# Kernel tuning notes

Measured on AMD Instinct MI355X. Metric: run time of the kernel, lower is better.

Reference implementation:

```python
import jax, jax.numpy as jnp
import numpy as np

B, N, E, NREG, DIN, F = 16, 20000, 640000, 2000, 128, 32
NEG_SLOPE = 0.2  # PyG GATConv default negative_slope


def setup_inputs() -> dict:
    key = jax.random.key(0)
    ks = jax.random.split(key, 10)
    x = jax.random.normal(ks[0], (B, N, DIN), dtype=jnp.float32)
    edge_src = jnp.sort(jax.random.randint(ks[1], (E,), 0, NREG, dtype=jnp.int64))
    edge_dst = jax.random.randint(ks[2], (E,), 0, N, dtype=jnp.int64)
    edge_attr = jax.random.uniform(ks[3], (B, E, 1), dtype=jnp.float32)
    # GATConv parameters (heads=1, concat=False, edge_dim=1)
    W = jax.random.normal(ks[4], (DIN, F), dtype=jnp.float32) * 0.05   # lin (shared src/dst)
    att_src = jax.random.normal(ks[5], (F,), dtype=jnp.float32) * 0.1
    att_dst = jax.random.normal(ks[6], (F,), dtype=jnp.float32) * 0.1
    lin_edge = jax.random.normal(ks[7], (1, F), dtype=jnp.float32) * 0.1
    att_edge = jax.random.normal(ks[8], (F,), dtype=jnp.float32) * 0.1
    bias = jax.random.normal(ks[9], (F,), dtype=jnp.float32) * 0.01
    return {"x": x, "edge_attr": edge_attr, "W": W, "att_src": att_src,
            "att_dst": att_dst, "lin_edge": lin_edge, "att_edge": att_edge,
            "bias": bias, "edge_src": edge_src, "edge_dst": edge_dst}


def _gat_regulon(x, eattr, W, att_src, att_dst, lin_edge, att_edge, bias,
                 src, dst):
    # x: [N, DIN], eattr: [E, 1]; src/dst: [E] int (src < NREG, sorted)
    h = x @ W                                  # [N, F]
    a_src = h @ att_src                        # [N]
    a_dst = h @ att_dst                        # [N]
    # add_self_loops=True with fill_value='mean' for edge_attr
    loop_attr = jnp.broadcast_to(jnp.mean(eattr, axis=0, keepdims=True), (N, 1))
    eattr_full = jnp.concatenate([eattr, loop_attr], axis=0)         # [E+N, 1]
    sl = jnp.arange(N, dtype=src.dtype)
    src_f = jnp.concatenate([src, sl])                               # [E+N]
    dst_f = jnp.concatenate([dst, sl])                               # [E+N]
    a_edge = (eattr_full @ lin_edge) @ att_edge                      # [E+N]
    alpha = jax.nn.leaky_relu(a_src[src_f] + a_dst[dst_f] + a_edge, NEG_SLOPE)
    # segment softmax over destination nodes (self-loops => no empty segment)
    m = jax.ops.segment_max(alpha, dst_f, num_segments=N)
    ex = jnp.exp(alpha - m[dst_f])
    s = jax.ops.segment_sum(ex, dst_f, num_segments=N)
    coef = ex / s[dst_f]                                             # [E+N]
    rep = jax.ops.segment_sum(coef[:, None] * h[src_f], dst_f, num_segments=N)
    rep = rep + bias                                                 # [N, F]
    # fused regulon pooling: out[i] = rep[i] + sum_{(i->t) in E} rep[t]
    pooled = jax.ops.segment_sum(rep[dst], src, num_segments=NREG)   # [NREG, F]
    return rep[:NREG] + pooled


def reference(x, edge_attr, W, att_src, att_dst, lin_edge, att_edge, bias,
              edge_src, edge_dst):
    fn = jax.vmap(lambda xi, ei: _gat_regulon(xi, ei, W, att_src, att_dst,
                                              lin_edge, att_edge, bias,
                                              edge_src, edge_dst))
    return fn(x, edge_attr)                                          # [B, NREG, F]
```

## Files before the change

### kernel.cpp

```cpp
#include <hip/hip_runtime.h>
#include <math.h>

#define B    16
#define N    20000
#define E    640000
#define NREG 2000
#define DIN  128
#define F    32
#define NEG  0.2f
#define BF   (B * F)
#define NCHUNK 8
#define CS   2500

typedef unsigned int uint;

__device__ inline uint bf16pair(float a, float b) {
    uint ua = __float_as_uint(a); ua = (ua + 0x7fffu + ((ua >> 16) & 1u)) >> 16;
    uint ub = __float_as_uint(b); ub = (ub + 0x7fffu + ((ub >> 16) & 1u)) >> 16;
    return ua | (ub << 16);
}
__device__ inline float bf16lo(uint v) { return __uint_as_float(v << 16); }
__device__ inline float bf16hi(uint v) { return __uint_as_float(v & 0xffff0000u); }

__global__ void k_hist(const int* __restrict__ dst, int* __restrict__ counts) {
    int e = blockIdx.x * blockDim.x + threadIdx.x;
    int stride = gridDim.x * blockDim.x;
    for (; e < E; e += stride)
        atomicAdd(&counts[dst[e]], 1);
}

__global__ void k_roff(const int* __restrict__ esrc, int* __restrict__ roff) {
    int r = blockIdx.x * blockDim.x + threadIdx.x;
    if (r > NREG) return;
    int lo = 0, hi = E;
    while (lo < hi) {
        int mid = (lo + hi) >> 1;
        if (esrc[mid] < r) lo = mid + 1; else hi = mid;
    }
    roff[r] = lo;
}

__global__ void k_scan(const int* __restrict__ in, int* __restrict__ out, int n) {
    __shared__ int sh[1024];
    int t = threadIdx.x;
    int chunk = (n + 1023) / 1024;
    int lo = t * chunk;
    int hi = lo + chunk; if (hi > n) hi = n;
    int local = 0;
    for (int i = lo; i < hi; ++i) local += in[i];
    sh[t] = local;
    __syncthreads();
    for (int d = 1; d < 1024; d <<= 1) {
        int v = (t >= d) ? sh[t - d] : 0;
        __syncthreads();
        sh[t] += v;
        __syncthreads();
    }
    int run = (t == 0) ? 0 : sh[t - 1];
    for (int i = lo; i < hi; ++i) { out[i] = run; run += in[i]; }
    if (t == 1023) out[n] = sh[1023];
}

__global__ void k_scatter(const int* __restrict__ src, const int* __restrict__ dst,
                          const int* __restrict__ off, int* __restrict__ cursor,
                          int* __restrict__ csr_src, int* __restrict__ pos_of_e) {
    int e = blockIdx.x * blockDim.x + threadIdx.x;
    int stride = gridDim.x * blockDim.x;
    for (; e < E; e += stride) {
        int d = dst[e];
        int pos = off[d] + atomicAdd(&cursor[d], 1);
        csr_src[pos] = src[e];
        pos_of_e[e] = pos;
    }
}

__global__ __launch_bounds__(256) void k_bucket(const int* __restrict__ edst,
                                                const int* __restrict__ roff,
                                                int* __restrict__ boff,
                                                int* __restrict__ pe_dst) {
    __shared__ int cnt[NCHUNK], pref[NCHUNK], cur[NCHUNK];
    int r = blockIdx.x;
    int t = threadIdx.x;
    int lo = roff[r], hi = roff[r + 1];
    if (t < NCHUNK) { cnt[t] = 0; cur[t] = 0; }
    __syncthreads();
    for (int e = lo + t; e < hi; e += 256)
        atomicAdd(&cnt[edst[e] / CS], 1);
    __syncthreads();
    if (t == 0) {
        int run = 0;
        #pragma unroll
        for (int c = 0; c < NCHUNK; ++c) { pref[c] = run; run += cnt[c]; }
    }
    __syncthreads();
    if (t < NCHUNK) boff[r * NCHUNK + t] = lo + pref[t];
    if (r == 0 && t == 0) boff[NREG * NCHUNK] = E;
    for (int e = lo + t; e < hi; e += 256) {
        int d = edst[e];
        int c = d / CS;
        int pos = lo + pref[c] + atomicAdd(&cur[c], 1);
        pe_dst[pos] = d;
    }
}

#define MEAN_BLOCKS_PER_B 64
__global__ void k_mean(const float* __restrict__ eattr, float* __restrict__ meanb) {
    int b   = blockIdx.x / MEAN_BLOCKS_PER_B;
    int blk = blockIdx.x % MEAN_BLOCKS_PER_B;
    int per = (E + MEAN_BLOCKS_PER_B - 1) / MEAN_BLOCKS_PER_B;
    int lo = blk * per;
    int hi = lo + per; if (hi > E) hi = E;
    float s = 0.f;
    for (int i = lo + threadIdx.x; i < hi; i += blockDim.x)
        s += eattr[(size_t)b * E + i];
    __shared__ float sh[256];
    sh[threadIdx.x] = s;
    __syncthreads();
    for (int d = 128; d > 0; d >>= 1) {
        if (threadIdx.x < d) sh[threadIdx.x] += sh[threadIdx.x + d];
        __syncthreads();
    }
    if (threadIdx.x == 0) atomicAdd(&meanb[b], sh[0]);
}

__global__ void k_cedge(const float* __restrict__ lin_edge,
                        const float* __restrict__ att_edge, float* __restrict__ c) {
    if (threadIdx.x == 0) {
        float s = 0.f;
        for (int f = 0; f < F; ++f) s += lin_edge[f] * att_edge[f];
        *c = s;
    }
}

__global__ __launch_bounds__(256) void k_edgew(const float* __restrict__ eattr,
                                               const int* __restrict__ esrc,
                                               const int* __restrict__ edst,
                                               const int* __restrict__ pos_of_e,
                                               const float* __restrict__ a_src,
                                               const float* __restrict__ a_dst,
                                               const float* __restrict__ cedge,
                                               float* __restrict__ wbuf) {
    __shared__ float tile[B][257];
    __shared__ int ssrc[256], sdst[256], spos[256];
    int e0 = blockIdx.x * 256;
    int t = threadIdx.x;
    #pragma unroll
    for (int b = 0; b < B; ++b)
        tile[b][t] = eattr[(size_t)b * E + e0 + t];
    ssrc[t] = esrc[e0 + t];
    sdst[t] = edst[e0 + t];
    spos[t] = pos_of_e[e0 + t];
    __syncthreads();
    float c = *cedge;
    #pragma unroll
    for (int p = 0; p < 16; ++p) {
        int idx = p * 256 + t;
        int el = idx >> 4;
        int bb = idx & 15;
        float a = a_src[(size_t)ssrc[el] * B + bb]
                + a_dst[(size_t)sdst[el] * B + bb]
                + tile[bb][el] * c;
        a = a > 0.f ? a : NEG * a;
        wbuf[(size_t)spos[el] * B + bb] = __expf(a);
    }
}

#define XS_LD 260
__global__ __launch_bounds__(256) void k_gemm(const float* __restrict__ x,
                                              const float* __restrict__ W,
                                              const float* __restrict__ att_src,
                                              const float* __restrict__ att_dst,
                                              uint* __restrict__ hu,
                                              float* __restrict__ a_src,
                                              float* __restrict__ a_dst) {
    __shared__ float Ws[DIN * F];
    __shared__ float xs[32 * XS_LD];
    int t = threadIdx.x;
    int row0 = blockIdx.x * 256;
    #pragma unroll
    for (int j = 0; j < 4; ++j) {
        int idx = (t + 256 * j) * 4;
        *(float4*)&Ws[idx] = *(const float4*)&W[idx];
    }
    const int lr = t & 63;
    const int fg = t >> 6;
    float acc[4][8];
    #pragma unroll
    for (int i = 0; i < 4; ++i)
        #pragma unroll
        for (int j = 0; j < 8; ++j) acc[i][j] = 0.f;

    for (int kc = 0; kc < 4; ++kc) {
        __syncthreads();
        #pragma unroll
        for (int j = 0; j < 8; ++j) {
            int p = t + 256 * j;
            int row = p >> 3;
            int kk  = (p & 7) * 4;
            float4 g = *(const float4*)&x[(size_t)(row0 + row) * DIN + kc * 32 + kk];
            xs[(kk + 0) * XS_LD + row] = g.x;
            xs[(kk + 1) * XS_LD + row] = g.y;
            xs[(kk + 2) * XS_LD + row] = g.z;
            xs[(kk + 3) * XS_LD + row] = g.w;
        }
        __syncthreads();
        #pragma unroll
        for (int k = 0; k < 32; ++k) {
            float4 xv = *(float4*)&xs[k * XS_LD + 4 * lr];
            float4 w0 = *(float4*)&Ws[(kc * 32 + k) * F + fg * 8];
            float4 w1 = *(float4*)&Ws[(kc * 32 + k) * F + fg * 8 + 4];
            float xr[4] = {xv.x, xv.y, xv.z, xv.w};
            float wr[8] = {w0.x, w0.y, w0.z, w0.w, w1.x, w1.y, w1.z, w1.w};
            #pragma unroll
            for (int i = 0; i < 4; ++i)
                #pragma unroll
                for (int j = 0; j < 8; ++j)
                    acc[i][j] = fmaf(xr[i], wr[j], acc[i][j]);
        }
    }
    #pragma unroll
    for (int i = 0; i < 4; ++i) {
        int row = row0 + lr * 4 + i;
        int b = row / N;
        int n = row - b * N;
        uint4 o;
        o.x = bf16pair(acc[i][0], acc[i][1]);
        o.y = bf16pair(acc[i][2], acc[i][3]);
        o.z = bf16pair(acc[i][4], acc[i][5]);
        o.w = bf16pair(acc[i][6], acc[i][7]);
        *(uint4*)&hu[(size_t)n * 256 + b * 16 + fg * 4] = o;
    }
    float* red = xs;
    __syncthreads();
    #pragma unroll
    for (int i = 0; i < 4; ++i) {
        float s1 = 0.f, s2 = 0.f;
        #pragma unroll
        for (int j = 0; j < 8; ++j) {
            float as = att_src[fg * 8 + j];
            float ad = att_dst[fg * 8 + j];
            s1 = fmaf(acc[i][j], as, s1);
            s2 = fmaf(acc[i][j], ad, s2);
        }
        red[fg * 256 + lr * 4 + i]        = s1;
        red[1024 + fg * 256 + lr * 4 + i] = s2;
    }
    __syncthreads();
    {
        float s1 = red[t] + red[256 + t] + red[512 + t] + red[768 + t];
        float s2 = red[1024 + t] + red[1280 + t] + red[1536 + t] + red[1792 + t];
        int row = row0 + t;
        int b = row / N;
        int n = row - b * N;
        a_src[(size_t)n * B + b] = s1;
        a_dst[(size_t)n * B + b] = s2;
    }
}

__global__ __launch_bounds__(256) void k_rep(
    const uint* __restrict__ hu, const float* __restrict__ a_src,
    const float* __restrict__ a_dst, const float* __restrict__ wbuf,
    const float* __restrict__ bias, const float* __restrict__ meanb,
    const float* __restrict__ cedge, const int* __restrict__ dst_off,
    const int* __restrict__ csr_src, uint* __restrict__ repu) {
    int i = blockIdx.x;
    int t = threadIdx.x;
    int b  = t >> 4;
    int fp = t & 15;
    float c = *cedge;
    float meanv = meanb[b] * (1.f / (float)E);
    float al = a_src[(size_t)i * B + b] + a_dst[(size_t)i * B + b] + meanv * c;
    al = al > 0.f ? al : NEG * al;
    float s = __expf(al);
    uint hv = hu[(size_t)i * 256 + t];
    float acc0 = s * bf16lo(hv);
    float acc1 = s * bf16hi(hv);
    int lo = dst_off[i], hi = dst_off[i + 1];
    int j = lo;
    for (; j + 4 <= hi; j += 4) {
        int s0 = csr_src[j], s1 = csr_src[j+1], s2 = csr_src[j+2], s3 = csr_src[j+3];
        float w0 = wbuf[(size_t)(j+0) * B + b];
        float w1 = wbuf[(size_t)(j+1) * B + b];
        float w2 = wbuf[(size_t)(j+2) * B + b];
        float w3 = wbuf[(size_t)(j+3) * B + b];
        uint v0 = hu[(size_t)s0 * 256 + t];
        uint v1 = hu[(size_t)s1 * 256 + t];
        uint v2 = hu[(size_t)s2 * 256 + t];
        uint v3 = hu[(size_t)s3 * 256 + t];
        s += w0 + w1 + w2 + w3;
        acc0 = fmaf(w0, bf16lo(v0), acc0);
        acc1 = fmaf(w0, bf16hi(v0), acc1);
        acc0 = fmaf(w1, bf16lo(v1), acc0);
        acc1 = fmaf(w1, bf16hi(v1), acc1);
        acc0 = fmaf(w2, bf16lo(v2), acc0);
        acc1 = fmaf(w2, bf16hi(v2), acc1);
        acc0 = fmaf(w3, bf16lo(v3), acc0);
        acc1 = fmaf(w3, bf16hi(v3), acc1);
    }
    for (; j < hi; ++j) {
        int sj = csr_src[j];
        float wv = wbuf[(size_t)j * B + b];
        uint v = hu[(size_t)sj * 256 + t];
        s += wv;
        acc0 = fmaf(wv, bf16lo(v), acc0);
        acc1 = fmaf(wv, bf16hi(v), acc1);
    }
    float inv = 1.f / s;
    repu[(size_t)i * 256 + t] = bf16pair(acc0 * inv + bias[2 * fp],
                                         acc1 * inv + bias[2 * fp + 1]);
}

__global__ __launch_bounds__(256) void k_pool(const uint* __restrict__ repu,
                                              const int* __restrict__ boff,
                                              const int* __restrict__ pe_dst,
                                              float* __restrict__ partial) {
    int key = blockIdx.x;
    int c = key / NREG;
    int r = key - c * NREG;
    int idx = r * NCHUNK + c;
    int t = threadIdx.x;
    int lo = boff[idx], hi = boff[idx + 1];
    float acc0 = 0.f, acc1 = 0.f;
    int e = lo;
    for (; e + 8 <= hi; e += 8) {
        int d0 = pe_dst[e+0], d1 = pe_dst[e+1], d2 = pe_dst[e+2], d3 = pe_dst[e+3];
        int d4 = pe_dst[e+4], d5 = pe_dst[e+5], d6 = pe_dst[e+6], d7 = pe_dst[e+7];
        uint v0 = repu[(size_t)d0 * 256 + t];
        uint v1 = repu[(size_t)d1 * 256 + t];
        uint v2 = repu[(size_t)d2 * 256 + t];
        uint v3 = repu[(size_t)d3 * 256 + t];
        uint v4 = repu[(size_t)d4 * 256 + t];
        uint v5 = repu[(size_t)d5 * 256 + t];
        uint v6 = repu[(size_t)d6 * 256 + t];
        uint v7 = repu[(size_t)d7 * 256 + t];
        acc0 += (bf16lo(v0) + bf16lo(v1)) + (bf16lo(v2) + bf16lo(v3))
              + (bf16lo(v4) + bf16lo(v5)) + (bf16lo(v6) + bf16lo(v7));
        acc1 += (bf16hi(v0) + bf16hi(v1)) + (bf16hi(v2) + bf16hi(v3))
              + (bf16hi(v4) + bf16hi(v5)) + (bf16hi(v6) + bf16hi(v7));
    }
    for (; e < hi; ++e) {
        int d = pe_dst[e];
        uint v = repu[(size_t)d * 256 + t];
        acc0 += bf16lo(v);
        acc1 += bf16hi(v);
    }
    float2 o = {acc0, acc1};
    *(float2*)&partial[((size_t)r * NCHUNK + c) * BF + 2 * t] = o;
}

__global__ __launch_bounds__(256) void k_combine(const uint* __restrict__ repu,
                                                 const float* __restrict__ partial,
                                                 float* __restrict__ out) {
    int r = blockIdx.x;
    int t = threadIdx.x;
    int b  = t >> 4;
    int fp = t & 15;
    uint v = repu[(size_t)r * 256 + t];
    float s0 = bf16lo(v), s1 = bf16hi(v);
    #pragma unroll
    for (int c = 0; c < NCHUNK; ++c) {
        float2 p = *(const float2*)&partial[((size_t)r * NCHUNK + c) * BF + 2 * t];
        s0 += p.x; s1 += p.y;
    }
    float2 o = {s0, s1};
    *(float2*)&out[(size_t)b * NREG * F + r * F + 2 * fp] = o;
}

extern "C" void kernel_launch(void* const* d_in, const int* in_sizes, int n_in,
                              void* d_out, int out_size, void* d_ws, size_t ws_size,
                              hipStream_t stream) {
    const float* x        = (const float*)d_in[0];
    const float* eattr    = (const float*)d_in[1];
    const float* W        = (const float*)d_in[2];
    const float* att_src  = (const float*)d_in[3];
    const float* att_dst  = (const float*)d_in[4];
    const float* lin_edge = (const float*)d_in[5];
    const float* att_edge = (const float*)d_in[6];
    const float* bias     = (const float*)d_in[7];
    const int*   esrc     = (const int*)d_in[8];
    const int*   edst     = (const int*)d_in[9];
    float* out = (float*)d_out;

    char* ws = (char*)d_ws;
    size_t off = 0;
    auto alloc = [&](size_t bytes) -> void* {
        void* p = ws + off;
        off = (off + bytes + 255) & ~(size_t)255;
        return p;
    };
    uint*  hu    = (uint*)alloc((size_t)N * 256 * 4);
    uint*  repu  = (uint*)alloc((size_t)N * 256 * 4);
    float* wbuf  = (float*)alloc((size_t)E * B * 4);
    float* a_src = (float*)alloc((size_t)N * B * 4);
    float* a_dst = (float*)alloc((size_t)N * B * 4);
    int* dst_off = (int*)alloc((size_t)(N + 1) * 4);
    int* roff    = (int*)alloc((size_t)(NREG + 1) * 4);
    int* csr_src = (int*)alloc((size_t)E * 4);
    int* pos_of_e= (int*)alloc((size_t)E * 4);
    int* pe_dst  = (int*)alloc((size_t)E * 4);
    int* boff    = (int*)alloc((size_t)(NREG * NCHUNK + 1) * 4);
    char* zbase   = ws + off;
    int* counts   = (int*)alloc((size_t)N * 4);
    int* cursor   = (int*)alloc((size_t)N * 4);
    float* meanb  = (float*)alloc((size_t)B * 4);
    float* cedge  = (float*)alloc(4);
    size_t zbytes = (size_t)((ws + off) - zbase);
    float* partial = wbuf;

    hipMemsetAsync(zbase, 0, zbytes, stream);

    k_hist<<<1024, 256, 0, stream>>>(edst, counts);
    k_scan<<<1, 1024, 0, stream>>>(counts, dst_off, N);
    k_roff<<<(NREG + 256) / 256, 256, 0, stream>>>(esrc, roff);
    k_scatter<<<1024, 256, 0, stream>>>(esrc, edst, dst_off, cursor,
                                        csr_src, pos_of_e);
    k_bucket<<<NREG, 256, 0, stream>>>(edst, roff, boff, pe_dst);
    k_mean<<<B * MEAN_BLOCKS_PER_B, 256, 0, stream>>>(eattr, meanb);
    k_cedge<<<1, 64, 0, stream>>>(lin_edge, att_edge, cedge);
    k_gemm<<<(B * N) / 256, 256, 0, stream>>>(x, W, att_src, att_dst,
                                              hu, a_src, a_dst);
    k_edgew<<<E / 256, 256, 0, stream>>>(eattr, esrc, edst, pos_of_e,
                                         a_src, a_dst, cedge, wbuf);
    k_rep<<<N, 256, 0, stream>>>(hu, a_src, a_dst, wbuf, bias, meanb, cedge,
                                 dst_off, csr_src, repu);
    k_pool<<<NREG * NCHUNK, 256, 0, stream>>>(repu, boff, pe_dst, partial);
    k_combine<<<NREG, 256, 0, stream>>>(repu, partial, out);
}
```

Before: 556.1 us.

## Fuse CSR scatter with edge-weight computation and store weights as bf16

Merges the CSR scatter and edge-weight kernels so each edge computes its exp-logits and writes them directly at its CSR slot, which removes the pos_of_e buffer and a separate pass. Edge weights are packed to bf16 (16 per edge in two uint4 stores), halving weight traffic for the later aggregation kernel, which now unrolls by 8 and reads packed weights. The roff and cedge launches are merged into one small kernel, and partial gets its own buffer instead of aliasing wbuf. bf16 weights lower the precision of the softmax numerator and denominator.

```diff
diff --git a/kernel.cpp b/kernel.cpp
--- a/kernel.cpp
+++ b/kernel.cpp
@@ -13,6 +13,7 @@
 #define CS   2500
 
 typedef unsigned int uint;
+typedef unsigned short ushort;
 
 __device__ inline uint bf16pair(float a, float b) {
     uint ua = __float_as_uint(a); ua = (ua + 0x7fffu + ((ua >> 16) & 1u)) >> 16;
@@ -27,17 +28,6 @@
     int stride = gridDim.x * blockDim.x;
     for (; e < E; e += stride)
         atomicAdd(&counts[dst[e]], 1);
-}
-
-__global__ void k_roff(const int* __restrict__ esrc, int* __restrict__ roff) {
-    int r = blockIdx.x * blockDim.x + threadIdx.x;
-    if (r > NREG) return;
-    int lo = 0, hi = E;
-    while (lo < hi) {
-        int mid = (lo + hi) >> 1;
-        if (esrc[mid] < r) lo = mid + 1; else hi = mid;
-    }
-    roff[r] = lo;
 }
 
 __global__ void k_scan(const int* __restrict__ in, int* __restrict__ out, int n) {
@@ -61,45 +51,24 @@
     if (t == 1023) out[n] = sh[1023];
 }
 
-__global__ void k_scatter(const int* __restrict__ src, const int* __restrict__ dst,
-                          const int* __restrict__ off, int* __restrict__ cursor,
-                          int* __restrict__ csr_src, int* __restrict__ pos_of_e) {
-    int e = blockIdx.x * blockDim.x + threadIdx.x;
-    int stride = gridDim.x * blockDim.x;
-    for (; e < E; e += stride) {
-        int d = dst[e];
-        int pos = off[d] + atomicAdd(&cursor[d], 1);
-        csr_src[pos] = src[e];
-        pos_of_e[e] = pos;
-    }
-}
-
-__global__ __launch_bounds__(256) void k_bucket(const int* __restrict__ edst,
-                                                const int* __restrict__ roff,
-                                                int* __restrict__ boff,
-                                                int* __restrict__ pe_dst) {
-    __shared__ int cnt[NCHUNK], pref[NCHUNK], cur[NCHUNK];
-    int r = blockIdx.x;
-    int t = threadIdx.x;
-    int lo = roff[r], hi = roff[r + 1];
-    if (t < NCHUNK) { cnt[t] = 0; cur[t] = 0; }
-    __syncthreads();
-    for (int e = lo + t; e < hi; e += 256)
-        atomicAdd(&cnt[edst[e] / CS], 1);
-    __syncthreads();
+__global__ __launch_bounds__(1024) void k_small(const int* __restrict__ esrc,
+                                                const float* __restrict__ lin_edge,
+                                                const float* __restrict__ att_edge,
+                                                int* __restrict__ roff,
+                                                float* __restrict__ cedge) {
+    int t = threadIdx.x;
+    for (int r = t; r <= NREG; r += 1024) {
+        int lo = 0, hi = E;
+        while (lo < hi) {
+            int mid = (lo + hi) >> 1;
+            if (esrc[mid] < r) lo = mid + 1; else hi = mid;
+        }
+        roff[r] = lo;
+    }
     if (t == 0) {
-        int run = 0;
-        #pragma unroll
-        for (int c = 0; c < NCHUNK; ++c) { pref[c] = run; run += cnt[c]; }
-    }
-    __syncthreads();
-    if (t < NCHUNK) boff[r * NCHUNK + t] = lo + pref[t];
-    if (r == 0 && t == 0) boff[NREG * NCHUNK] = E;
-    for (int e = lo + t; e < hi; e += 256) {
-        int d = edst[e];
-        int c = d / CS;
-        int pos = lo + pref[c] + atomicAdd(&cur[c], 1);
-        pe_dst[pos] = d;
+        float s = 0.f;
+        for (int f = 0; f < F; ++f) s += lin_edge[f] * att_edge[f];
+        *cedge = s;
     }
 }
 
@@ -123,48 +92,6 @@
     if (threadIdx.x == 0) atomicAdd(&meanb[b], sh[0]);
 }
 
-__global__ void k_cedge(const float* __restrict__ lin_edge,
-                        const float* __restrict__ att_edge, float* __restrict__ c) {
-    if (threadIdx.x == 0) {
-        float s = 0.f;
-        for (int f = 0; f < F; ++f) s += lin_edge[f] * att_edge[f];
-        *c = s;
-    }
-}
-
-__global__ __launch_bounds__(256) void k_edgew(const float* __restrict__ eattr,
-                                               const int* __restrict__ esrc,
-                                               const int* __restrict__ edst,
-                                               const int* __restrict__ pos_of_e,
-                                               const float* __restrict__ a_src,
-                                               const float* __restrict__ a_dst,
-                                               const float* __restrict__ cedge,
-                                               float* __restrict__ wbuf) {
-    __shared__ float tile[B][257];
-    __shared__ int ssrc[256], sdst[256], spos[256];
-    int e0 = blockIdx.x * 256;
-    int t = threadIdx.x;
-    #pragma unroll
-    for (int b = 0; b < B; ++b)
-        tile[b][t] = eattr[(size_t)b * E + e0 + t];
-    ssrc[t] = esrc[e0 + t];
-    sdst[t] = edst[e0 + t];
-    spos[t] = pos_of_e[e0 + t];
-    __syncthreads();
-    float c = *cedge;
-    #pragma unroll
-    for (int p = 0; p < 16; ++p) {
-        int idx = p * 256 + t;
-        int el = idx >> 4;
-        int bb = idx & 15;
-        float a = a_src[(size_t)ssrc[el] * B + bb]
-                + a_dst[(size_t)sdst[el] * B + bb]
-                + tile[bb][el] * c;
-        a = a > 0.f ? a : NEG * a;
-        wbuf[(size_t)spos[el] * B + bb] = __expf(a);
-    }
-}
-
 #define XS_LD 260
 __global__ __launch_bounds__(256) void k_gemm(const float* __restrict__ x,
                                               const float* __restrict__ W,
@@ -257,9 +184,73 @@
     }
 }
 
+__global__ __launch_bounds__(256) void k_scatedge(
+    const int* __restrict__ esrc, const int* __restrict__ edst,
+    const int* __restrict__ dst_off, int* __restrict__ cursor,
+    const float* __restrict__ eattr, const float* __restrict__ a_src,
+    const float* __restrict__ a_dst, const float* __restrict__ cedge,
+    int* __restrict__ csr_src, uint* __restrict__ wbuf16) {
+    int e = blockIdx.x * blockDim.x + threadIdx.x;
+    int s = esrc[e];
+    int d = edst[e];
+    int pos = dst_off[d] + atomicAdd(&cursor[d], 1);
+    csr_src[pos] = s;
+    float c = *cedge;
+    float4 as[4], ad[4];
+    #pragma unroll
+    for (int q = 0; q < 4; ++q) {
+        as[q] = *(const float4*)&a_src[(size_t)s * B + 4 * q];
+        ad[q] = *(const float4*)&a_dst[(size_t)d * B + 4 * q];
+    }
+    float w[16];
+    #pragma unroll
+    for (int b = 0; b < B; ++b) {
+        float ea = eattr[(size_t)b * E + e];
+        float a = ((const float*)as)[b] + ((const float*)ad)[b] + ea * c;
+        a = a > 0.f ? a : NEG * a;
+        w[b] = __expf(a);
+    }
+    uint4 o0, o1;
+    o0.x = bf16pair(w[0],  w[1]);  o0.y = bf16pair(w[2],  w[3]);
+    o0.z = bf16pair(w[4],  w[5]);  o0.w = bf16pair(w[6],  w[7]);
+    o1.x = bf16pair(w[8],  w[9]);  o1.y = bf16pair(w[10], w[11]);
+    o1.z = bf16pair(w[12], w[13]); o1.w = bf16pair(w[14], w[15]);
+    *(uint4*)&wbuf16[(size_t)pos * 8]     = o0;
+    *(uint4*)&wbuf16[(size_t)pos * 8 + 4] = o1;
+}
+
+__global__ __launch_bounds__(256) void k_bucket(const int* __restrict__ edst,
+                                                const int* __restrict__ roff,
+                                                int* __restrict__ boff,
+                                                int* __restrict__ pe_dst) {
+    __shared__ int cnt[NCHUNK], pref[NCHUNK], cur[NCHUNK];
+    int r = blockIdx.x;
+    int t = threadIdx.x;
+    int lo = roff[r], hi = roff[r + 1];
+    if (t < NCHUNK) { cnt[t] = 0; cur[t] = 0; }
+    __syncthreads();
+    for (int e = lo + t; e < hi; e += 256)
+        atomicAdd(&cnt[edst[e] / CS], 1);
+    __syncthreads();
+    if (t == 0) {
+        int run = 0;
+        #pragma unroll
+        for (int c = 0; c < NCHUNK; ++c) { pref[c] = run; run += cnt[c]; }
+    }
+    __syncthreads();
+    if (t < NCHUNK) boff[r * NCHUNK + t] = lo + pref[t];
+    if (r == 0 && t == 0) boff[NREG * NCHUNK] = E;
+    for (int e = lo + t; e < hi; e += 256) {
+        int d = edst[e];
+        int c = d / CS;
+        int pos = lo + pref[c] + atomicAdd(&cur[c], 1);
+        pe_dst[pos] = d;
+    }
+}
+
 __global__ __launch_bounds__(256) void k_rep(
     const uint* __restrict__ hu, const float* __restrict__ a_src,
-    const float* __restrict__ a_dst, const float* __restrict__ wbuf,
+    const float* __restrict__ a_dst, const uint* __restrict__ wbuf16,
     const float* __restrict__ bias, const float* __restrict__ meanb,
     const float* __restrict__ cedge, const int* __restrict__ dst_off,
     const int* __restrict__ csr_src, uint* __restrict__ repu) {
@@ -267,6 +258,8 @@
     int t = threadIdx.x;
     int b  = t >> 4;
     int fp = t & 15;
+    int bh = b >> 1;
+    int bl = b & 1;
     float c = *cedge;
     float meanv = meanb[b] * (1.f / (float)E);
     float al = a_src[(size_t)i * B + b] + a_dst[(size_t)i * B + b] + meanv * c;
@@ -277,33 +270,34 @@
     float acc1 = s * bf16hi(hv);
     int lo = dst_off[i], hi = dst_off[i + 1];
     int j = lo;
-    for (; j + 4 <= hi; j += 4) {
-        int s0 = csr_src[j], s1 = csr_src[j+1], s2 = csr_src[j+2], s3 = csr_src[j+3];
-        float w0 = wbuf[(size_t)(j+0) * B + b];
-        float w1 = wbuf[(size_t)(j+1) * B + b];
-        float w2 = wbuf[(size_t)(j+2) * B + b];
-        float w3 = wbuf[(size_t)(j+3) * B + b];
-        uint v0 = hu[(size_t)s0 * 256 + t];
-        uint v1 = hu[(size_t)s1 * 256 + t];
-        uint v2 = hu[(size_t)s2 * 256 + t];
-        uint v3 = hu[(size_t)s3 * 256 + t];
-        s += w0 + w1 + w2 + w3;
-        acc0 = fmaf(w0, bf16lo(v0), acc0);
-        acc1 = fmaf(w0, bf16hi(v0), acc1);
-        acc0 = fmaf(w1, bf16lo(v1), acc0);
-        acc1 = fmaf(w1, bf16hi(v1), acc1);
-        acc0 = fmaf(w2, bf16lo(v2), acc0);
-        acc1 = fmaf(w2, bf16hi(v2), acc1);
-        acc0 = fmaf(w3, bf16lo(v3), acc0);
-        acc1 = fmaf(w3, bf16hi(v3), acc1);
+    for (; j + 8 <= hi; j += 8) {
+        int   sx[8];
+        float wx[8];
+        uint  vx[8];
+        #pragma unroll
+        for (int q = 0; q < 8; ++q) sx[q] = csr_src[j + q];
+        #pragma unroll
+        for (int q = 0; q < 8; ++q) {
+            uint wv = wbuf16[(size_t)(j + q) * 8 + bh];
+            wx[q] = bl ? bf16hi(wv) : bf16lo(wv);
+        }
+        #pragma unroll
+        for (int q = 0; q < 8; ++q) vx[q] = hu[(size_t)sx[q] * 256 + t];
+        #pragma unroll
+        for (int q = 0; q < 8; ++q) {
+            s += wx[q];
+            acc0 = fmaf(wx[q], bf16lo(vx[q]), acc0);
+            acc1 = fmaf(wx[q], bf16hi(vx[q]), acc1);
+        }
     }
     for (; j < hi; ++j) {
         int sj = csr_src[j];
-        float wv = wbuf[(size_t)j * B + b];
+        uint wv = wbuf16[(size_t)j * 8 + bh];
+        float w = bl ? bf16hi(wv) : bf16lo(wv);
         uint v = hu[(size_t)sj * 256 + t];
-        s += wv;
-        acc0 = fmaf(wv, bf16lo(v), acc0);
-        acc1 = fmaf(wv, bf16hi(v), acc1);
+        s += w;
+        acc0 = fmaf(w, bf16lo(v), acc0);
+        acc1 = fmaf(w, bf16hi(v), acc1);
     }
     float inv = 1.f / s;
     repu[(size_t)i * 256 + t] = bf16pair(acc0 * inv + bias[2 * fp],
@@ -388,40 +382,37 @@
         off = (off + bytes + 255) & ~(size_t)255;
         return p;
     };
-    uint*  hu    = (uint*)alloc((size_t)N * 256 * 4);
-    uint*  repu  = (uint*)alloc((size_t)N * 256 * 4);
-    float* wbuf  = (float*)alloc((size_t)E * B * 4);
-    float* a_src = (float*)alloc((size_t)N * B * 4);
-    float* a_dst = (float*)alloc((size_t)N * B * 4);
-    int* dst_off = (int*)alloc((size_t)(N + 1) * 4);
-    int* roff    = (int*)alloc((size_t)(NREG + 1) * 4);
-    int* csr_src = (int*)alloc((size_t)E * 4);
-    int* pos_of_e= (int*)alloc((size_t)E * 4);
-    int* pe_dst  = (int*)alloc((size_t)E * 4);
-    int* boff    = (int*)alloc((size_t)(NREG * NCHUNK + 1) * 4);
+    uint*  hu     = (uint*)alloc((size_t)N * 256 * 4);
+    uint*  repu   = (uint*)alloc((size_t)N * 256 * 4);
+    uint*  wbuf16 = (uint*)alloc((size_t)E * 8 * 4);
+    float* partial= (float*)alloc((size_t)NREG * NCHUNK * BF * 4);
+    float* a_src  = (float*)alloc((size_t)N * B * 4);
+    float* a_dst  = (float*)alloc((size_t)N * B * 4);
+    int* dst_off  = (int*)alloc((size_t)(N + 1) * 4);
+    int* roff     = (int*)alloc((size_t)(NREG + 1) * 4);
+    int* csr_src  = (int*)alloc((size_t)E * 4);
+    int* pe_dst   = (int*)alloc((size_t)E * 4);
+    int* boff     = (int*)alloc((size_t)(NREG * NCHUNK + 1) * 4);
     char* zbase   = ws + off;
     int* counts   = (int*)alloc((size_t)N * 4);
     int* cursor   = (int*)alloc((size_t)N * 4);
     float* meanb  = (float*)alloc((size_t)B * 4);
     float* cedge  = (float*)alloc(4);
     size_t zbytes = (size_t)((ws + off) - zbase);
-    float* partial = wbuf;
 
     hipMemsetAsync(zbase, 0, zbytes, stream);
 
     k_hist<<<1024, 256, 0, stream>>>(edst, counts);
     k_scan<<<1, 1024, 0, stream>>>(counts, dst_off, N);
-    k_roff<<<(NREG + 256) / 256, 256, 0, stream>>>(esrc, roff);
-    k_scatter<<<1024, 256, 0, stream>>>(esrc, edst, dst_off, cursor,
-                                        csr_src, pos_of_e);
-    k_bucket<<<NREG, 256, 0, stream>>>(edst, roff, boff, pe_dst);
+    k_small<<<1, 1024, 0, stream>>>(esrc, lin_edge, att_edge, roff, cedge);
     k_mean<<<B * MEAN_BLOCKS_PER_B, 256, 0, stream>>>(eattr, meanb);
-    k_cedge<<<1, 64, 0, stream>>>(lin_edge, att_edge, cedge);
     k_gemm<<<(B * N) / 256, 256, 0, stream>>>(x, W, att_src, att_dst,
                                               hu, a_src, a_dst);
-    k_edgew<<<E / 256, 256, 0, stream>>>(eattr, esrc, edst, pos_of_e,
-                                         a_src, a_dst, cedge, wbuf);
-    k_rep<<<N, 256, 0, stream>>>(hu, a_src, a_dst, wbuf, bias, meanb, cedge,
+    k_scatedge<<<E / 256, 256, 0, stream>>>(esrc, edst, dst_off, cursor,
+                                            eattr, a_src, a_dst, cedge,
+                                            csr_src, wbuf16);
+    k_bucket<<<NREG, 256, 0, stream>>>(edst, roff, boff, pe_dst);
+    k_rep<<<N, 256, 0, stream>>>(hu, a_src, a_dst, wbuf16, bias, meanb, cedge,
                                  dst_off, csr_src, repu);
     k_pool<<<NREG * NCHUNK, 256, 0, stream>>>(repu, boff, pe_dst, partial);
     k_combine<<<NREG, 256, 0, stream>>>(repu, partial, out);
```

New measurement: 558.7 us. Within noise of the previous version (+0.5%).
